# Performance work log

Hardware: AMD Instinct MI355X
Metric: run time of the kernel (lower is better)

Reference implementation:

```python
import jax, jax.numpy as jnp
import numpy as np

D_MODEL = 1024
NHEAD = 16
HEAD_DIM = D_MODEL // NHEAD
B, S = 8, 1024
NEG = -1e9  # finite stand-in for -inf (same softmax result, grad-safe)


def setup_inputs() -> dict:
    key = jax.random.key(0)
    ks = jax.random.split(key, 12)
    sc = 1.0 / np.sqrt(D_MODEL)
    inp = {
        "q": jax.random.normal(ks[0], (B, S, D_MODEL), jnp.float32),
        "k": jax.random.normal(ks[1], (B, S, D_MODEL), jnp.float32),
        "v": jax.random.normal(ks[2], (B, S, D_MODEL), jnp.float32),
        "padding_mask": jax.random.bernoulli(ks[3], 0.1, (B, S)),
        "causal_mask": jnp.where(jnp.tril(jnp.ones((S, S), bool)), 0.0, NEG).astype(jnp.float32),
        "wq": jax.random.normal(ks[4], (D_MODEL, D_MODEL), jnp.float32) * sc,
        "bq": jax.random.normal(ks[5], (D_MODEL,), jnp.float32) * sc,
        "wk": jax.random.normal(ks[6], (D_MODEL, D_MODEL), jnp.float32) * sc,
        "wv": jax.random.normal(ks[7], (D_MODEL, D_MODEL), jnp.float32) * sc,
        "bv": jax.random.normal(ks[8], (D_MODEL,), jnp.float32) * sc,
        "wo": jax.random.normal(ks[9], (D_MODEL, D_MODEL), jnp.float32) * sc,
        "bo": jax.random.normal(ks[10], (D_MODEL,), jnp.float32) * sc,
    }
    return inp


def reference(q, k, v, padding_mask, causal_mask, wq, bq, wk, wv, bv, wo, bo):
    b = q.shape[0]
    # projections (torch Linear: x @ W.T + b); k_linear has no bias
    qp = q @ wq.T + bq
    kp = k @ wk.T
    vp = v @ wv.T + bv
    # [B, S, H, Dh] -> [B, H, S, Dh]
    qh = qp.reshape(b, -1, NHEAD, HEAD_DIM).transpose(0, 2, 1, 3)
    kh = kp.reshape(b, -1, NHEAD, HEAD_DIM).transpose(0, 2, 1, 3)
    vh = vp.reshape(b, -1, NHEAD, HEAD_DIM).transpose(0, 2, 1, 3)
    scores = jnp.einsum("bhqd,bhkd->bhqk", qh, kh) / np.sqrt(HEAD_DIM).astype(np.float32)
    scores = jnp.where(padding_mask[:, None, None, :], NEG, scores)
    scores = scores + causal_mask[None, None, :, :]
    attn = jax.nn.softmax(scores, axis=-1)
    out = jnp.einsum("bhqk,bhkd->bhqd", attn, vh)
    out = out.transpose(0, 2, 1, 3).reshape(b, -1, D_MODEL)
    return out @ wo.T + bo
```

## Files before the change

### kernel.cpp

```cpp
#include <hip/hip_runtime.h>
#include <hip/hip_bf16.h>
#include <cstdint>
#include <math.h>


typedef __bf16 bf16_t;
typedef __bf16 bf16x8 __attribute__((ext_vector_type(8)));
typedef __bf16 bf16x4 __attribute__((ext_vector_type(4)));
typedef float  f32x4  __attribute__((ext_vector_type(4)));

#define MFMA16(a, b, c) __builtin_amdgcn_mfma_f32_16x16x32_bf16((a), (b), (c), 0, 0, 0)
#define NEGV (-1e9f)

__device__ __forceinline__ void gl_lds16(const void* gp, void* lp) {
  __builtin_amdgcn_global_load_lds(
      (__attribute__((address_space(1))) void*)(gp),
      (__attribute__((address_space(3))) void*)(lp), 16, 0, 0);
}

__device__ __forceinline__ void bar() {
  asm volatile("" ::: "memory");
  __builtin_amdgcn_s_barrier();
  asm volatile("" ::: "memory");
}

__device__ __forceinline__ unsigned int pk2(float lo, float hi) {
  unsigned short a = __builtin_bit_cast(unsigned short, (bf16_t)lo);
  unsigned short b = __builtin_bit_cast(unsigned short, (bf16_t)hi);
  return (unsigned int)a | ((unsigned int)b << 16);
}

__device__ __forceinline__ void cvt_body(const float* __restrict__ in,
                                         bf16_t* __restrict__ out, int i) {
  const float4* p = reinterpret_cast<const float4*>(in) + (size_t)i * 2;
  float4 a = p[0], b = p[1];
  bf16x8 r = {(bf16_t)a.x, (bf16_t)a.y, (bf16_t)a.z, (bf16_t)a.w,
              (bf16_t)b.x, (bf16_t)b.y, (bf16_t)b.z, (bf16_t)b.w};
  *reinterpret_cast<bf16x8*>(out + (size_t)i * 8) = r;
}

__global__ __launch_bounds__(256) void cvt_all(
    const float* __restrict__ q, const float* __restrict__ k, const float* __restrict__ v,
    const float* __restrict__ wq, const float* __restrict__ wk,
    const float* __restrict__ wv, const float* __restrict__ wo,
    bf16_t* __restrict__ oq, bf16_t* __restrict__ ok, bf16_t* __restrict__ ov,
    bf16_t* __restrict__ owq, bf16_t* __restrict__ owk,
    bf16_t* __restrict__ owv, bf16_t* __restrict__ owo) {
  const int bid = (int)blockIdx.x;
  if (bid < 12288) {
    const int s = bid >> 12;
    const int i = (bid & 4095) * 256 + (int)threadIdx.x;
    cvt_body(s == 0 ? q : (s == 1 ? k : v),
             s == 0 ? oq : (s == 1 ? ok : ov), i);
  } else {
    const int r = bid - 12288;
    const int s = r >> 9;
    const int i = (r & 511) * 256 + (int)threadIdx.x;
    cvt_body(s == 0 ? wq : (s == 1 ? wk : (s == 2 ? wv : wo)),
             s == 0 ? owq : (s == 1 ? owk : (s == 2 ? owv : owo)), i);
  }
}

__global__ __launch_bounds__(512, 4) void gemm_qkv(const bf16_t* __restrict__ qbf,
                                                   const bf16_t* __restrict__ kbf,
                                                   const bf16_t* __restrict__ vbf,
                                                   const bf16_t* __restrict__ wqb,
                                                   const bf16_t* __restrict__ wkb,
                                                   const bf16_t* __restrict__ wvb,
                                                   const float* __restrict__ bq,
                                                   const float* __restrict__ bv,
                                                   bf16_t* __restrict__ qp,
                                                   bf16_t* __restrict__ kp,
                                                   bf16_t* __restrict__ vtw) {
  __shared__ __align__(16) char lds[73728];
  const int bid = (int)blockIdx.x;
  const int z = bid >> 8;
  const int idx = bid & 255;
  const int p = ((idx >> 6) << 3) | (idx & 7);
  const int n = (idx >> 3) & 7;
  const bf16_t* A = z == 0 ? qbf : (z == 1 ? kbf : vbf);
  const bf16_t* W = z == 0 ? wqb : (z == 1 ? wkb : wvb);
  const int t = threadIdx.x;
  const int w = t >> 6, l = t & 63, lr = l & 15, lg = l >> 4;
  const int wr = w >> 1, wc = w & 1;
  const int m0 = p * 256, n0 = n * 128;
  const int K = 1024, N = 1024;

  const int gc = (t & 3) ^ ((t >> 3) & 3);
  const bf16_t* Ag = A + (size_t)(m0 + (t >> 2)) * K + gc * 8;
  const bf16_t* Wg = W + (size_t)(n0 + (t >> 2)) * K + gc * 8;

  auto stageA = [&](int buf, int tile) {
    char* dst = lds + buf * 16384 + t * 16;
    const size_t kt = (size_t)tile * 32;
    gl_lds16(Ag + kt,                   dst);
    gl_lds16(Ag + kt + (size_t)128 * K, dst + 8192);
  };
  auto stageB = [&](int buf, int tile) {
    gl_lds16(Wg + (size_t)tile * 32, lds + 49152 + buf * 8192 + t * 16);
  };

  stageA(0, 0); stageB(0, 0); stageA(1, 1); stageB(1, 1);
  asm volatile("s_waitcnt vmcnt(3)" ::: "memory");
  bar();

  f32x4 acc[4][4] = {};
  const int cofs = (lg ^ ((lr >> 1) & 3)) << 4;

  for (int T = 0; T < 32; ++T) {
    const int cur = T % 3;
    const char* Ab = lds + cur * 16384;
    const char* Bb = lds + 49152 + cur * 8192;
    bf16x8 af[4], bfr[4];
#pragma unroll
    for (int mt = 0; mt < 4; mt++)
      af[mt] = *(const bf16x8*)(Ab + (wr * 64 + mt * 16 + lr) * 64 + cofs);
#pragma unroll
    for (int nt = 0; nt < 4; nt++)
      bfr[nt] = *(const bf16x8*)(Bb + (wc * 64 + nt * 16 + lr) * 64 + cofs);
    if (T + 2 < 32) { stageA((T + 2) % 3, T + 2); stageB((T + 2) % 3, T + 2); }
    if (T < 30)       asm volatile("s_waitcnt vmcnt(3)" ::: "memory");
    else if (T == 30) asm volatile("s_waitcnt vmcnt(0)" ::: "memory");
    bar();
    asm volatile("s_waitcnt lgkmcnt(0)" ::: "memory");
    __builtin_amdgcn_s_setprio(1);
#pragma unroll
    for (int mt = 0; mt < 4; mt++)
#pragma unroll
      for (int nt = 0; nt < 4; nt++)
        acc[mt][nt] = MFMA16(af[mt], bfr[nt], acc[mt][nt]);
    __builtin_amdgcn_s_setprio(0);
    bar();
  }

  if (z != 2) {
    bf16_t* outp = (z == 0) ? qp : kp;
    const float sc = (z == 0) ? 0.125f : 1.0f;
#pragma unroll
    for (int nt = 0; nt < 4; nt++) {
      const int col = n0 + wc * 64 + nt * 16 + lr;
      const float bb = (z == 0) ? bq[col] : 0.0f;
#pragma unroll
      for (int mt = 0; mt < 4; mt++)
#pragma unroll
        for (int i = 0; i < 4; i++) {
          const int row = m0 + wr * 64 + mt * 16 + lg * 4 + i;
          outp[(size_t)row * N + col] = (bf16_t)((acc[mt][nt][i] + bb) * sc);
        }
    }
  } else {
    __syncthreads();
    char* Tl = lds;
#pragma unroll
    for (int nt = 0; nt < 4; nt++) {
      const int col_l = wc * 64 + nt * 16 + lr;
      const float bb = bv[n0 + col_l];
#pragma unroll
      for (int mt = 0; mt < 4; mt++)
#pragma unroll
        for (int i = 0; i < 4; i++) {
          const int row_l = wr * 64 + mt * 16 + lg * 4 + i;
          *(bf16_t*)(Tl + col_l * 512 + ((row_l * 2) ^ ((col_l & 7) << 4))) =
              (bf16_t)(acc[mt][nt][i] + bb);
        }
    }
    __syncthreads();
    const int b = m0 >> 10, s0 = m0 & 1023;
    const int c_l = t >> 2, sub = t & 3;
    bf16_t* dst = vtw + (size_t)(b * 1024 + n0 + c_l) * 1024 + s0 + sub * 64;
    const char* Trow = Tl + c_l * 512;
    const int sw2 = (c_l & 7) << 4;
#pragma unroll
    for (int jj = 0; jj < 8; jj++) {
      const int lc = sub * 8 + jj;
      bf16x8 vv = *(const bf16x8*)(Trow + ((lc << 4) ^ sw2));
      *(bf16x8*)(dst + jj * 8) = vv;
    }
  }
}

__global__ __launch_bounds__(512) void gemm_out(const bf16_t* __restrict__ A,
                                                const bf16_t* __restrict__ W,
                                                const float* __restrict__ bias,
                                                float* __restrict__ outp) {
  __shared__ __align__(16) char lds[147456];
  const int bid = (int)blockIdx.x;
  const int p = ((bid >> 6) << 3) | (bid & 7);
  const int n = (bid >> 3) & 7;
  const int t = threadIdx.x;
  const int w = t >> 6, l = t & 63, lr = l & 15, lg = l >> 4;
  const int wr = w >> 1, wc = w & 1;
  const int m0 = p * 256, n0 = n * 128;
  const int K = 1024, N = 1024;

  const int gc = (t & 7) ^ ((t >> 3) & 7);
  const bf16_t* Ag = A + (size_t)(m0 + (t >> 3)) * K + gc * 8;
  const bf16_t* Wg = W + (size_t)(n0 + (t >> 3)) * K + gc * 8;

  auto stageA = [&](int buf, int tile) {
    char* dst = lds + buf * 32768 + t * 16;
    const size_t kt = (size_t)tile * 64;
    gl_lds16(Ag + kt,                    dst);
    gl_lds16(Ag + kt + (size_t)64 * K,   dst + 8192);
    gl_lds16(Ag + kt + (size_t)128 * K,  dst + 16384);
    gl_lds16(Ag + kt + (size_t)192 * K,  dst + 24576);
  };
  auto stageB = [&](int buf, int tile) {
    char* dst = lds + 98304 + buf * 16384 + t * 16;
    const size_t kt = (size_t)tile * 64;
    gl_lds16(Wg + kt,                    dst);
    gl_lds16(Wg + kt + (size_t)64 * K,   dst + 8192);
  };
  stageA(0, 0); stageB(0, 0); stageA(1, 1); stageB(1, 1);
  asm volatile("s_waitcnt vmcnt(6)" ::: "memory");
  bar();

  f32x4 acc[4][4] = {};
  const int xorv = (lr & 7) << 4;
  const int k0o = lg * 16, k1o = 64 + lg * 16;

  for (int T = 0; T < 16; ++T) {
    const int cur = T % 3;
    const char* Ab = lds + cur * 32768;
    const char* Bb = lds + 98304 + cur * 16384;
    bf16x8 af[4][2], b0[2][2], b1[2][2];
#pragma unroll
    for (int mt = 0; mt < 4; mt++) {
      const int row = wr * 64 + mt * 16 + lr;
      af[mt][0] = *(const bf16x8*)(Ab + row * 128 + (k0o ^ xorv));
      af[mt][1] = *(const bf16x8*)(Ab + row * 128 + (k1o ^ xorv));
    }
#pragma unroll
    for (int nt = 0; nt < 2; nt++) {
      const int row = wc * 64 + nt * 16 + lr;
      b0[nt][0] = *(const bf16x8*)(Bb + row * 128 + (k0o ^ xorv));
      b0[nt][1] = *(const bf16x8*)(Bb + row * 128 + (k1o ^ xorv));
    }
    if (T + 2 < 16) stageA((T + 2) % 3, T + 2);
    bar();
    asm volatile("s_waitcnt lgkmcnt(0)" ::: "memory");
    __builtin_amdgcn_s_setprio(1);
#pragma unroll
    for (int mt = 0; mt < 4; mt++)
#pragma unroll
      for (int nt = 0; nt < 2; nt++) {
        acc[mt][nt] = MFMA16(af[mt][0], b0[nt][0], acc[mt][nt]);
        acc[mt][nt] = MFMA16(af[mt][1], b0[nt][1], acc[mt][nt]);
      }
    __builtin_amdgcn_s_setprio(0);
    bar();
#pragma unroll
    for (int nt = 0; nt < 2; nt++) {
      const int row = wc * 64 + (nt + 2) * 16 + lr;
      b1[nt][0] = *(const bf16x8*)(Bb + row * 128 + (k0o ^ xorv));
      b1[nt][1] = *(const bf16x8*)(Bb + row * 128 + (k1o ^ xorv));
    }
    if (T + 2 < 16) stageB((T + 2) % 3, T + 2);
    if (T < 14)       asm volatile("s_waitcnt vmcnt(6)" ::: "memory");
    else if (T == 14) asm volatile("s_waitcnt vmcnt(0)" ::: "memory");
    bar();
    asm volatile("s_waitcnt lgkmcnt(0)" ::: "memory");
    __builtin_amdgcn_s_setprio(1);
#pragma unroll
    for (int mt = 0; mt < 4; mt++)
#pragma unroll
      for (int nt = 0; nt < 2; nt++) {
        acc[mt][nt + 2] = MFMA16(af[mt][0], b1[nt][0], acc[mt][nt + 2]);
        acc[mt][nt + 2] = MFMA16(af[mt][1], b1[nt][1], acc[mt][nt + 2]);
      }
    __builtin_amdgcn_s_setprio(0);
    bar();
  }

#pragma unroll
  for (int nt = 0; nt < 4; nt++) {
    const int col = n0 + wc * 64 + nt * 16 + lr;
    const float bb = bias[col];
#pragma unroll
    for (int mt = 0; mt < 4; mt++)
#pragma unroll
      for (int i = 0; i < 4; i++) {
        const int row = m0 + wr * 64 + mt * 16 + lg * 4 + i;
        outp[(size_t)row * N + col] = acc[mt][nt][i] + bb;
      }
  }
}

__device__ __forceinline__ void pack_bfly(const f32x4 (&s)[4], int lg,
                                          bf16x8& pbv0, bf16x8& pbv1) {
  unsigned int u[4][2], sh[4][2];
#pragma unroll
  for (int nt = 0; nt < 4; nt++) {
    u[nt][0] = pk2(s[nt][0], s[nt][1]);
    u[nt][1] = pk2(s[nt][2], s[nt][3]);
  }
#pragma unroll
  for (int nt = 0; nt < 4; nt++) {
    sh[nt][0] = (unsigned int)__shfl_xor((int)u[nt][0], 16, 64);
    sh[nt][1] = (unsigned int)__shfl_xor((int)u[nt][1], 16, 64);
  }
  const bool ev = (lg & 1) == 0;
  unsigned int Y[8];
  Y[0] = ev ? u[0][0] : sh[1][0];  Y[1] = ev ? u[0][1] : sh[1][1];
  Y[2] = ev ? u[2][0] : sh[3][0];  Y[3] = ev ? u[2][1] : sh[3][1];
  Y[4] = ev ? sh[0][0] : u[1][0];  Y[5] = ev ? sh[0][1] : u[1][1];
  Y[6] = ev ? sh[2][0] : u[3][0];  Y[7] = ev ? sh[2][1] : u[3][1];
  const bool mid = (lg == 1) || (lg == 2);
#pragma unroll
  for (int j = 0; j < 8; j++) {
    const unsigned int z = (unsigned int)__shfl_xor((int)Y[j], 48, 64);
    Y[j] = mid ? z : Y[j];
  }
  union U8 { unsigned int u[4]; bf16x8 v; };
  U8 p0, p1;
  p0.u[0] = Y[0]; p0.u[1] = Y[1]; p0.u[2] = Y[4]; p0.u[3] = Y[5];
  p1.u[0] = Y[2]; p1.u[1] = Y[3]; p1.u[2] = Y[6]; p1.u[3] = Y[7];
  pbv0 = p0.v;
  pbv1 = p1.v;
}

__global__ __launch_bounds__(512, 8) void attn_fused(const bf16_t* __restrict__ qp,
                                                     const bf16_t* __restrict__ kp,
                                                     const bf16_t* __restrict__ vt,
                                                     const int* __restrict__ pad,
                                                     bf16_t* __restrict__ outp) {
  __shared__ bf16_t Ks[2][64 * 64];
  __shared__ bf16_t Vts[2][64 * 64];
  __shared__ int padI[1024];
  __shared__ int sfl[8], sfh[8];
  const int t = threadIdx.x, w = t >> 6, l = t & 63, lr = l & 15, lg = l >> 4;
  const int L = (int)blockIdx.x;
  const int bh = (L & 7) + ((L >> 6) << 3);
  const int j = (L >> 3) & 7;
  const int b = bh >> 4, h = bh & 15;
  const int lo = j, hi = 15 - j;

  const int srow = t >> 3, sc = t & 7;
  const int gc = sc ^ (srow & 7);
  const bf16_t* kgb = kp + (size_t)(b * 1024 + srow) * 1024 + h * 64 + gc * 8;
  const bf16_t* vgb = vt + (size_t)(bh * 64 + srow) * 1024 + gc * 8;

  auto stage = [&](int bufi, int k0s) {
    gl_lds16(kgb + (size_t)k0s * 1024, (char*)(Ks[bufi]) + t * 16);
    gl_lds16(vgb + k0s,                (char*)(Vts[bufi]) + t * 16);
  };

  bool unl = false, unh = false;
  for (int jj = t; jj <= hi * 64; jj += 512) {
    const bool u = (pad[b * 1024 + jj] == 0);
    unh |= u;
    unl |= (u && (jj <= lo * 64));
  }
  const bool al = __any(unl), ah = __any(unh);
  if (l == 0) { sfl[w] = al ? 1 : 0; sfh[w] = ah ? 1 : 0; }

  stage(0, 0);
  if (t < 256) gl_lds16(pad + b * 1024 + t * 4, (char*)padI + t * 16);

  const int mytile = (w < 4) ? hi : lo;
  const int qrow_l = mytile * 64 + (w & 3) * 16 + lr;
  const int base16 = mytile * 64 + (w & 3) * 16;
  const bf16_t* qg = qp + (size_t)(b * 1024 + qrow_l) * 1024 + h * 64 + lg * 8;
  const bf16x8 qa0 = *reinterpret_cast<const bf16x8*>(qg);
  const bf16x8 qa1 = *reinterpret_cast<const bf16x8*>(qg + 32);

  __syncthreads();
  int ul = 0, uh = 0;
#pragma unroll
  for (int i = 0; i < 8; i++) { ul |= sfl[i]; uh |= sfh[i]; }
  const bool mydeg = (w < 4) ? (uh == 0) : (ul == 0);
  const int ktEnd = (ul == 0) ? 16 : (hi + 1);

  f32x4 o[4] = {};
  float m_ = -INFINITY, ld_ = 0.0f;

  for (int kt = 0; kt < ktEnd; ++kt) {
    const int cur = kt & 1;
    if (kt + 1 < ktEnd) {
      stage(cur ^ 1, (kt + 1) * 64);
      asm volatile("s_waitcnt vmcnt(2)" ::: "memory");
    } else {
      asm volatile("s_waitcnt vmcnt(0)" ::: "memory");
    }
    __builtin_amdgcn_s_barrier();

    if (kt <= mytile || mydeg) {
      const char* Kb = (const char*)(Ks[cur]);
      const char* Vb = (const char*)(Vts[cur]);
      const int k0 = kt * 64;

      f32x4 s[4] = {};
#pragma unroll
      for (int nt = 0; nt < 4; nt++) {
        const int row = nt * 16 + lr;
        const int sw = (row & 7) << 4;
        bf16x8 kb0 = *reinterpret_cast<const bf16x8*>(Kb + row * 128 + ((lg * 16) ^ sw));
        bf16x8 kb1 = *reinterpret_cast<const bf16x8*>(Kb + row * 128 + ((lg * 16 + 64) ^ sw));
        s[nt] = MFMA16(kb0, qa0, s[nt]);
        s[nt] = MFMA16(kb1, qa1, s[nt]);
      }

      const bool nc = (k0 + 63 > base16);
#pragma unroll
      for (int nt = 0; nt < 4; nt++) {
        const int kc4 = k0 + nt * 16 + lg * 4;
        const int4 pd = *reinterpret_cast<const int4*>(&padI[kc4]);
        const int pdv[4] = {pd.x, pd.y, pd.z, pd.w};
#pragma unroll
        for (int i = 0; i < 4; i++) {
          float v = s[nt][i];
          if (pdv[i]) v = NEGV;
          if (nc && (kc4 + i > qrow_l)) v += NEGV;
          s[nt][i] = v;
        }
      }

      float mx = s[0][0];
#pragma unroll
      for (int nt = 0; nt < 4; nt++)
#pragma unroll
        for (int i = 0; i < 4; i++) mx = fmaxf(mx, s[nt][i]);
      mx = fmaxf(mx, __shfl_xor(mx, 16, 64));
      mx = fmaxf(mx, __shfl_xor(mx, 32, 64));

      if (!__all(mx <= m_ - 88.0f)) {
        if (!__all(mx <= m_ + 8.0f)) {
          const float mn = fmaxf(m_, mx);
          const float scl = __expf(m_ - mn);
          m_ = mn;
          ld_ *= scl;
#pragma unroll
          for (int nt = 0; nt < 4; nt++) o[nt] *= scl;
        }
        float a = 0.0f;
#pragma unroll
        for (int nt = 0; nt < 4; nt++)
#pragma unroll
          for (int i = 0; i < 4; i++) {
            const float p = __expf(s[nt][i] - m_);
            s[nt][i] = p;
            a += p;
          }
        a += __shfl_xor(a, 16, 64);
        a += __shfl_xor(a, 32, 64);
        ld_ += a;

        bf16x8 pb0, pb1;
        pack_bfly(s, lg, pb0, pb1);

#pragma unroll
        for (int nt = 0; nt < 4; nt++) {
          const int vrow = nt * 16 + lr;
          const int vsw = (vrow & 7) << 4;
          bf16x8 vf0 = *reinterpret_cast<const bf16x8*>(Vb + vrow * 128 + ((lg * 16) ^ vsw));
          bf16x8 vf1 = *reinterpret_cast<const bf16x8*>(Vb + vrow * 128 + ((64 + lg * 16) ^ vsw));
          o[nt] = MFMA16(vf0, pb0, o[nt]);
          o[nt] = MFMA16(vf1, pb1, o[nt]);
        }
      }
    }
    __builtin_amdgcn_s_barrier();
  }

  const float rinv = 1.0f / ld_;
#pragma unroll
  for (int nt = 0; nt < 4; nt++) {
    bf16x4 rr = {(bf16_t)(o[nt][0] * rinv), (bf16_t)(o[nt][1] * rinv),
                 (bf16_t)(o[nt][2] * rinv), (bf16_t)(o[nt][3] * rinv)};
    *reinterpret_cast<bf16x4*>(outp + (size_t)(b * 1024 + qrow_l) * 1024 + h * 64 + nt * 16 + lg * 4) = rr;
  }
}

extern "C" void kernel_launch(void* const* d_in, const int* in_sizes, int n_in,
                              void* d_out, int out_size, void* d_ws, size_t ws_size,
                              hipStream_t stream) {
  const float* q   = (const float*)d_in[0];
  const float* k   = (const float*)d_in[1];
  const float* v   = (const float*)d_in[2];
  const int*   pad = (const int*)d_in[3];
  const float* wq  = (const float*)d_in[5];
  const float* bq  = (const float*)d_in[6];
  const float* wk  = (const float*)d_in[7];
  const float* wv  = (const float*)d_in[8];
  const float* bv  = (const float*)d_in[9];
  const float* wo  = (const float*)d_in[10];
  const float* bo  = (const float*)d_in[11];

  char* ws = (char*)d_ws;
  const size_t MiB = 1024 * 1024;
  bf16_t* qbf = (bf16_t*)(ws + 0 * MiB);
  bf16_t* kbf = (bf16_t*)(ws + 16 * MiB);
  bf16_t* vbf = (bf16_t*)(ws + 32 * MiB);
  bf16_t* qp  = (bf16_t*)(ws + 48 * MiB);
  bf16_t* kp  = (bf16_t*)(ws + 64 * MiB);
  bf16_t* vtw = (bf16_t*)(ws + 80 * MiB);
  bf16_t* wqb = (bf16_t*)(ws + 96 * MiB);
  bf16_t* wkb = (bf16_t*)(ws + 98 * MiB);
  bf16_t* wvb = (bf16_t*)(ws + 100 * MiB);
  bf16_t* wob = (bf16_t*)(ws + 102 * MiB);
  bf16_t* attnO = qbf;

  cvt_all<<<14336, 256, 0, stream>>>(q, k, v, wq, wk, wv, wo,
                                     qbf, kbf, vbf, wqb, wkb, wvb, wob);

  gemm_qkv<<<768, 512, 0, stream>>>(qbf, kbf, vbf, wqb, wkb, wvb, bq, bv, qp, kp, vtw);

  attn_fused<<<1024, 512, 0, stream>>>(qp, kp, vtw, pad, attnO);

  gemm_out<<<256, 512, 0, stream>>>(attnO, wob, bo, (float*)d_out);
}
```

Baseline: 171.4 us.

## Assign contiguous 128-row query blocks per workgroup instead of paired lo/hi tiles

Replaces the balanced pairing of a low and a high 64-row query tile per workgroup with one contiguous 128-row query block per workgroup, with heaviest blocks launched first via reversed j. The number of key tiles each workgroup streams now depends on its block index (2j+2), so work per workgroup is no longer balanced. In exchange, the 8 waves share the same key range with less wasted staging: in the old scheme the low-tile waves sat idle while the high tile's keys streamed. Relies on longest-first ordering to smooth the tail imbalance.

```diff
diff --git a/kernel.cpp b/kernel.cpp
--- a/kernel.cpp
+++ b/kernel.cpp
@@ -327,13 +327,13 @@
   __shared__ bf16_t Ks[2][64 * 64];
   __shared__ bf16_t Vts[2][64 * 64];
   __shared__ int padI[1024];
-  __shared__ int sfl[8], sfh[8];
+  __shared__ int sf[8];
   const int t = threadIdx.x, w = t >> 6, l = t & 63, lr = l & 15, lg = l >> 4;
   const int L = (int)blockIdx.x;
   const int bh = (L & 7) + ((L >> 6) << 3);
-  const int j = (L >> 3) & 7;
+  const int j = 7 - ((L >> 3) & 7);
   const int b = bh >> 4, h = bh & 15;
-  const int lo = j, hi = 15 - j;
+  const int q0 = j * 128;
 
   const int srow = t >> 3, sc = t & 7;
   const int gc = sc ^ (srow & 7);
@@ -345,31 +345,26 @@
     gl_lds16(vgb + k0s,                (char*)(Vts[bufi]) + t * 16);
   };
 
-  bool unl = false, unh = false;
-  for (int jj = t; jj <= hi * 64; jj += 512) {
-    const bool u = (pad[b * 1024 + jj] == 0);
-    unh |= u;
-    unl |= (u && (jj <= lo * 64));
-  }
-  const bool al = __any(unl), ah = __any(unh);
-  if (l == 0) { sfl[w] = al ? 1 : 0; sfh[w] = ah ? 1 : 0; }
+  bool un = false;
+  for (int jj = t; jj <= q0; jj += 512) un |= (pad[b * 1024 + jj] == 0);
+  const bool anyun = __any(un);
+  if (l == 0) sf[w] = anyun ? 1 : 0;
 
   stage(0, 0);
   if (t < 256) gl_lds16(pad + b * 1024 + t * 4, (char*)padI + t * 16);
 
-  const int mytile = (w < 4) ? hi : lo;
-  const int qrow_l = mytile * 64 + (w & 3) * 16 + lr;
-  const int base16 = mytile * 64 + (w & 3) * 16;
+  const int base16 = q0 + w * 16;
+  const int qrow_l = base16 + lr;
+  const int myend = (base16 + 15) >> 6;
   const bf16_t* qg = qp + (size_t)(b * 1024 + qrow_l) * 1024 + h * 64 + lg * 8;
   const bf16x8 qa0 = *reinterpret_cast<const bf16x8*>(qg);
   const bf16x8 qa1 = *reinterpret_cast<const bf16x8*>(qg + 32);
 
   __syncthreads();
-  int ul = 0, uh = 0;
-#pragma unroll
-  for (int i = 0; i < 8; i++) { ul |= sfl[i]; uh |= sfh[i]; }
-  const bool mydeg = (w < 4) ? (uh == 0) : (ul == 0);
-  const int ktEnd = (ul == 0) ? 16 : (hi + 1);
+  int ul = 0;
+#pragma unroll
+  for (int i = 0; i < 8; i++) ul |= sf[i];
+  const int ktEnd = ul ? (2 * j + 2) : 16;
 
   f32x4 o[4] = {};
   float m_ = -INFINITY, ld_ = 0.0f;
@@ -384,7 +379,7 @@
     }
     __builtin_amdgcn_s_barrier();
 
-    if (kt <= mytile || mydeg) {
+    if (kt <= myend || !ul) {
       const char* Kb = (const char*)(Ks[cur]);
       const char* Vb = (const char*)(Vts[cur]);
       const int k0 = kt * 64;
```

Measured after the change: 189.8 us. 10.8% more time.

## Shrink output GEMM tile to 128x128 with K=32 stages; prioritize attention MFMAs

Applied to the files above, without the earlier changes.

The output projection GEMM moves from 512-thread blocks on 256x128 tiles with K=64 stages to 256-thread blocks on 128x128 tiles with K=32 stages. That doubles the grid to 512 blocks, cuts LDS to 48KB so two blocks can fit per CU, and changes the swizzle to suit 64-byte rows. Its aim is better occupancy and wave coverage across the CUs, at the cost of more loop iterations, more barriers and less operand reuse per block. Separately, the attention kernel raises wave priority around its QK and PV MFMA blocks so matrix work is favored over other waves.

```diff
diff --git a/kernel.cpp b/kernel.cpp
--- a/kernel.cpp
+++ b/kernel.cpp
@@ -179,95 +179,66 @@
   }
 }
 
-__global__ __launch_bounds__(512) void gemm_out(const bf16_t* __restrict__ A,
-                                                const bf16_t* __restrict__ W,
-                                                const float* __restrict__ bias,
-                                                float* __restrict__ outp) {
-  __shared__ __align__(16) char lds[147456];
+__global__ __launch_bounds__(256, 2) void gemm_out(const bf16_t* __restrict__ A,
+                                                   const bf16_t* __restrict__ W,
+                                                   const float* __restrict__ bias,
+                                                   float* __restrict__ outp) {
+  __shared__ __align__(16) char lds[49152];
   const int bid = (int)blockIdx.x;
   const int p = ((bid >> 6) << 3) | (bid & 7);
   const int n = (bid >> 3) & 7;
   const int t = threadIdx.x;
   const int w = t >> 6, l = t & 63, lr = l & 15, lg = l >> 4;
   const int wr = w >> 1, wc = w & 1;
-  const int m0 = p * 256, n0 = n * 128;
+  const int m0 = p * 128, n0 = n * 128;
   const int K = 1024, N = 1024;
 
-  const int gc = (t & 7) ^ ((t >> 3) & 7);
-  const bf16_t* Ag = A + (size_t)(m0 + (t >> 3)) * K + gc * 8;
-  const bf16_t* Wg = W + (size_t)(n0 + (t >> 3)) * K + gc * 8;
+  const int gc = (t & 3) ^ ((t >> 3) & 3);
+  const bf16_t* Ag = A + (size_t)(m0 + (t >> 2)) * K + gc * 8;
+  const bf16_t* Wg = W + (size_t)(n0 + (t >> 2)) * K + gc * 8;
 
   auto stageA = [&](int buf, int tile) {
-    char* dst = lds + buf * 32768 + t * 16;
-    const size_t kt = (size_t)tile * 64;
-    gl_lds16(Ag + kt,                    dst);
-    gl_lds16(Ag + kt + (size_t)64 * K,   dst + 8192);
-    gl_lds16(Ag + kt + (size_t)128 * K,  dst + 16384);
-    gl_lds16(Ag + kt + (size_t)192 * K,  dst + 24576);
+    char* dst = lds + buf * 8192 + t * 16;
+    const size_t kt = (size_t)tile * 32;
+    gl_lds16(Ag + kt,                  dst);
+    gl_lds16(Ag + kt + (size_t)64 * K, dst + 4096);
   };
   auto stageB = [&](int buf, int tile) {
-    char* dst = lds + 98304 + buf * 16384 + t * 16;
-    const size_t kt = (size_t)tile * 64;
-    gl_lds16(Wg + kt,                    dst);
-    gl_lds16(Wg + kt + (size_t)64 * K,   dst + 8192);
+    char* dst = lds + 24576 + buf * 8192 + t * 16;
+    const size_t kt = (size_t)tile * 32;
+    gl_lds16(Wg + kt,                  dst);
+    gl_lds16(Wg + kt + (size_t)64 * K, dst + 4096);
   };
+
   stageA(0, 0); stageB(0, 0); stageA(1, 1); stageB(1, 1);
-  asm volatile("s_waitcnt vmcnt(6)" ::: "memory");
+  asm volatile("s_waitcnt vmcnt(4)" ::: "memory");
   bar();
 
   f32x4 acc[4][4] = {};
-  const int xorv = (lr & 7) << 4;
-  const int k0o = lg * 16, k1o = 64 + lg * 16;
-
-  for (int T = 0; T < 16; ++T) {
+  const int cofs = (lg ^ ((lr >> 1) & 3)) << 4;
+
+  for (int T = 0; T < 32; ++T) {
     const int cur = T % 3;
-    const char* Ab = lds + cur * 32768;
-    const char* Bb = lds + 98304 + cur * 16384;
-    bf16x8 af[4][2], b0[2][2], b1[2][2];
-#pragma unroll
-    for (int mt = 0; mt < 4; mt++) {
-      const int row = wr * 64 + mt * 16 + lr;
-      af[mt][0] = *(const bf16x8*)(Ab + row * 128 + (k0o ^ xorv));
-      af[mt][1] = *(const bf16x8*)(Ab + row * 128 + (k1o ^ xorv));
-    }
-#pragma unroll
-    for (int nt = 0; nt < 2; nt++) {
-      const int row = wc * 64 + nt * 16 + lr;
-      b0[nt][0] = *(const bf16x8*)(Bb + row * 128 + (k0o ^ xorv));
-      b0[nt][1] = *(const bf16x8*)(Bb + row * 128 + (k1o ^ xorv));
-    }
-    if (T + 2 < 16) stageA((T + 2) % 3, T + 2);
+    const char* Ab = lds + cur * 8192;
+    const char* Bb = lds + 24576 + cur * 8192;
+    bf16x8 af[4], bfr[4];
+#pragma unroll
+    for (int mt = 0; mt < 4; mt++)
+      af[mt] = *(const bf16x8*)(Ab + (wr * 64 + mt * 16 + lr) * 64 + cofs);
+#pragma unroll
+    for (int nt = 0; nt < 4; nt++)
+      bfr[nt] = *(const bf16x8*)(Bb + (wc * 64 + nt * 16 + lr) * 64 + cofs);
+    if (T + 2 < 32) { stageA((T + 2) % 3, T + 2); stageB((T + 2) % 3, T + 2); }
+    if (T < 30)       asm volatile("s_waitcnt vmcnt(4)" ::: "memory");
+    else if (T == 30) asm volatile("s_waitcnt vmcnt(0)" ::: "memory");
     bar();
     asm volatile("s_waitcnt lgkmcnt(0)" ::: "memory");
     __builtin_amdgcn_s_setprio(1);
 #pragma unroll
     for (int mt = 0; mt < 4; mt++)
 #pragma unroll
-      for (int nt = 0; nt < 2; nt++) {
-        acc[mt][nt] = MFMA16(af[mt][0], b0[nt][0], acc[mt][nt]);
-        acc[mt][nt] = MFMA16(af[mt][1], b0[nt][1], acc[mt][nt]);
-      }
-    __builtin_amdgcn_s_setprio(0);
-    bar();
-#pragma unroll
-    for (int nt = 0; nt < 2; nt++) {
-      const int row = wc * 64 + (nt + 2) * 16 + lr;
-      b1[nt][0] = *(const bf16x8*)(Bb + row * 128 + (k0o ^ xorv));
-      b1[nt][1] = *(const bf16x8*)(Bb + row * 128 + (k1o ^ xorv));
-    }
-    if (T + 2 < 16) stageB((T + 2) % 3, T + 2);
-    if (T < 14)       asm volatile("s_waitcnt vmcnt(6)" ::: "memory");
-    else if (T == 14) asm volatile("s_waitcnt vmcnt(0)" ::: "memory");
-    bar();
-    asm volatile("s_waitcnt lgkmcnt(0)" ::: "memory");
-    __builtin_amdgcn_s_setprio(1);
-#pragma unroll
-    for (int mt = 0; mt < 4; mt++)
-#pragma unroll
-      for (int nt = 0; nt < 2; nt++) {
-        acc[mt][nt + 2] = MFMA16(af[mt][0], b1[nt][0], acc[mt][nt + 2]);
-        acc[mt][nt + 2] = MFMA16(af[mt][1], b1[nt][1], acc[mt][nt + 2]);
-      }
+      for (int nt = 0; nt < 4; nt++)
+        acc[mt][nt] = MFMA16(af[mt], bfr[nt], acc[mt][nt]);
     __builtin_amdgcn_s_setprio(0);
     bar();
   }
@@ -390,6 +361,7 @@
       const int k0 = kt * 64;
 
       f32x4 s[4] = {};
+      __builtin_amdgcn_s_setprio(1);
 #pragma unroll
       for (int nt = 0; nt < 4; nt++) {
         const int row = nt * 16 + lr;
@@ -399,6 +371,7 @@
         s[nt] = MFMA16(kb0, qa0, s[nt]);
         s[nt] = MFMA16(kb1, qa1, s[nt]);
       }
+      __builtin_amdgcn_s_setprio(0);
 
       const bool nc = (k0 + 63 > base16);
 #pragma unroll
@@ -448,6 +421,7 @@
         bf16x8 pb0, pb1;
         pack_bfly(s, lg, pb0, pb1);
 
+        __builtin_amdgcn_s_setprio(1);
 #pragma unroll
         for (int nt = 0; nt < 4; nt++) {
           const int vrow = nt * 16 + lr;
@@ -457,6 +431,7 @@
           o[nt] = MFMA16(vf0, pb0, o[nt]);
           o[nt] = MFMA16(vf1, pb1, o[nt]);
         }
+        __builtin_amdgcn_s_setprio(0);
       }
     }
     __builtin_amdgcn_s_barrier();
@@ -507,5 +482,5 @@
 
   attn_fused<<<1024, 512, 0, stream>>>(qp, kp, vtw, pad, attnO);
 
-  gemm_out<<<256, 512, 0, stream>>>(attnO, wob, bo, (float*)d_out);
-}
+  gemm_out<<<512, 256, 0, stream>>>(attnO, wob, bo, (float*)d_out);
+}
```

Measured after the change: 171.2 us. Within noise of the previous version (-0.1%).
